# Kernel optimization log

Hardware: AMD Instinct MI355X
Metric: run time of the kernel (lower is better)

Reference implementation:

```python
import jax, jax.numpy as jnp
import numpy as np

N_EMBD = 768
N_HEAD = 12
HEAD_DIM = N_EMBD // N_HEAD
EPS = 1e-6


def setup_inputs() -> dict:
    key = jax.random.key(0)
    ks = jax.random.split(key, 8)
    B, T, C = 4, 2048, N_EMBD
    s = 0.02
    return {
        "x": jax.random.normal(ks[0], (B, T, C), jnp.float32),
        "ln1_w": jnp.ones((C,), jnp.float32),
        "ln1_b": jnp.zeros((C,), jnp.float32),
        "W_attn": jax.random.normal(ks[1], (C, 3 * C), jnp.float32) * s,
        "b_attn": jnp.zeros((3 * C,), jnp.float32),
        "W_attn_proj": jax.random.normal(ks[2], (C, C), jnp.float32) * s,
        "b_attn_proj": jnp.zeros((C,), jnp.float32),
        "ln2_w": jnp.ones((C,), jnp.float32),
        "ln2_b": jnp.zeros((C,), jnp.float32),
        "W_fc": jax.random.normal(ks[3], (C, 4 * C), jnp.float32) * s,
        "b_fc": jnp.zeros((4 * C,), jnp.float32),
        "W_mlp_proj": jax.random.normal(ks[4], (4 * C, C), jnp.float32) * s,
        "b_mlp_proj": jnp.zeros((C,), jnp.float32),
    }


def layer_norm(x, w, b):
    # Faithful to MyLayerNorm: (x - mean) / (std + eps), std with ddof=0
    mean = jnp.mean(x, axis=-1, keepdims=True)
    std = jnp.sqrt(jnp.mean((x - mean) ** 2, axis=-1, keepdims=True))
    return w * (x - mean) / (std + EPS) + b


def attention(h, W_attn, b_attn, W_proj, b_proj):
    B, T, C = h.shape
    qkv = h @ W_attn + b_attn                      # [B,T,3C]
    q, k, v = jnp.split(qkv, 3, axis=-1)
    # [B,T,C] -> [B,H,T,D]
    def to_heads(t):
        return t.reshape(B, T, N_HEAD, HEAD_DIM).transpose(0, 2, 1, 3)
    q, k, v = to_heads(q), to_heads(k), to_heads(v)
    att = jnp.einsum("bhtd,bhsd->bhts", q, k) * (1.0 / np.sqrt(HEAD_DIM))
    causal = jnp.tril(jnp.ones((T, T), bool))[None, None]
    att = jnp.where(causal, att, -jnp.inf)
    att = jax.nn.softmax(att, axis=-1)
    y = jnp.einsum("bhts,bhsd->bhtd", att, v)      # [B,H,T,D]
    y = y.transpose(0, 2, 1, 3).reshape(B, T, C)
    return y @ W_proj + b_proj


def mlp(h, W_fc, b_fc, W_proj, b_proj):
    h = jax.nn.gelu(h @ W_fc + b_fc, approximate=False)
    return h @ W_proj + b_proj


def reference(x, ln1_w, ln1_b, W_attn, b_attn, W_attn_proj, b_attn_proj,
              ln2_w, ln2_b, W_fc, b_fc, W_mlp_proj, b_mlp_proj):
    x = x + attention(layer_norm(x, ln1_w, ln1_b), W_attn, b_attn, W_attn_proj, b_attn_proj)
    x = x + mlp(layer_norm(x, ln2_w, ln2_b), W_fc, b_fc, W_mlp_proj, b_mlp_proj)
    return x
```

## Files before the change

### kernel.cpp

```cpp
#include <hip/hip_runtime.h>
#include <hip/hip_bf16.h>
#include <math.h>

#define N_EMBD 768
#define N_HEAD 12
#define HEAD_DIM 64
#define TOKENS 8192
#define SEQ 2048
#define BATCH 4
#define NQT (SEQ / 64)

typedef __attribute__((ext_vector_type(8))) short short8;
typedef __attribute__((ext_vector_type(4))) short short4v;
typedef __attribute__((ext_vector_type(4))) float f32x4;

__device__ __forceinline__ short f2bf(float f) {
    unsigned u = __builtin_bit_cast(unsigned, f);
    unsigned r = (u + 0x7fffu + ((u >> 16) & 1u)) >> 16;
    return (short)r;
}
__device__ __forceinline__ short f2bf_fast(float f) {
    unsigned u = __builtin_bit_cast(unsigned, f);
    return (short)((u + 0x8000u) >> 16);
}

__device__ __forceinline__ float gelu_fast(float x) {
    float z = 1.5957691216057308f * x * (1.0f + 0.044715f * x * x);
    return x / (1.0f + __expf(-z));
}

__device__ __forceinline__ void gld16(const void* g, void* l) {
    __builtin_amdgcn_global_load_lds(
        (const __attribute__((address_space(1))) unsigned int*)g,
        (__attribute__((address_space(3))) unsigned int*)l, 16, 0, 0);
}

__global__ __launch_bounds__(256) void wT_all(
        const float* __restrict__ Wa, short* __restrict__ Ta,
        const float* __restrict__ Wp, short* __restrict__ Tp,
        const float* __restrict__ Wf, short* __restrict__ Tf,
        const float* __restrict__ Wm, short* __restrict__ Tm) {
    __shared__ float T[32][33];
    int id = blockIdx.x;
    const float* W; short* Wt; int K, N;
    if (id < 1728)      { W = Wa; Wt = Ta; K = 768;  N = 2304; }
    else if (id < 2304) { W = Wp; Wt = Tp; K = 768;  N = 768;  id -= 1728; }
    else if (id < 4608) { W = Wf; Wt = Tf; K = 768;  N = 3072; id -= 2304; }
    else                { W = Wm; Wt = Tm; K = 3072; N = 768;  id -= 4608; }
    int tn = N >> 5;
    int n0 = (id % tn) * 32, k0 = (id / tn) * 32;
    int c = threadIdx.x & 31, r0 = threadIdx.x >> 5;
#pragma unroll
    for (int i = 0; i < 32; i += 8)
        T[r0 + i][c] = W[(size_t)(k0 + r0 + i) * N + n0 + c];
    __syncthreads();
#pragma unroll
    for (int i = 0; i < 32; i += 8)
        Wt[(size_t)(n0 + r0 + i) * K + k0 + c] = f2bf(T[c][r0 + i]);
}

__global__ __launch_bounds__(256) void ln_bf_kernel(const float* __restrict__ x,
                                                    const float* __restrict__ w,
                                                    const float* __restrict__ b,
                                                    short* __restrict__ out) {
    int row = blockIdx.x * 4 + (threadIdx.x >> 6);
    int lane = threadIdx.x & 63;
    const float4* xr = (const float4*)(x + (size_t)row * N_EMBD);
    const float4* wr = (const float4*)w;
    const float4* br = (const float4*)b;

    float4 v[3];
#pragma unroll
    for (int i = 0; i < 3; ++i) v[i] = xr[lane + 64 * i];
    float s = 0.f;
#pragma unroll
    for (int i = 0; i < 3; ++i) s += v[i].x + v[i].y + v[i].z + v[i].w;
#pragma unroll
    for (int off = 1; off < 64; off <<= 1) s += __shfl_xor(s, off, 64);
    float mean = s * (1.f / 768.f);

    float var = 0.f;
#pragma unroll
    for (int i = 0; i < 3; ++i) {
        float a0 = v[i].x - mean, a1 = v[i].y - mean,
              a2 = v[i].z - mean, a3 = v[i].w - mean;
        var += a0 * a0 + a1 * a1 + a2 * a2 + a3 * a3;
    }
#pragma unroll
    for (int off = 1; off < 64; off <<= 1) var += __shfl_xor(var, off, 64);
    float inv = 1.f / (sqrtf(var * (1.f / 768.f)) + 1e-6f);

    short4v* yr = (short4v*)(out + (size_t)row * N_EMBD);
#pragma unroll
    for (int i = 0; i < 3; ++i) {
        float4 wv = wr[lane + 64 * i], bv = br[lane + 64 * i];
        short4v o;
        o[0] = f2bf(wv.x * (v[i].x - mean) * inv + bv.x);
        o[1] = f2bf(wv.y * (v[i].y - mean) * inv + bv.y);
        o[2] = f2bf(wv.z * (v[i].z - mean) * inv + bv.z);
        o[3] = f2bf(wv.w * (v[i].w - mean) * inv + bv.w);
        yr[lane + 64 * i] = o;
    }
}

template <int ACT, int RES, int OUTBF, int VOUT>
__global__ __launch_bounds__(256) void gemm_mfma(
        const short* __restrict__ A,
        const short* __restrict__ Bt,
        const float* __restrict__ bias,
        const float* __restrict__ res,
        void* __restrict__ outp,
        short* __restrict__ vt,
        int M, int N, int K) {
    __shared__ short As[8192];
    __shared__ short Bs[8192];
    int tid = threadIdx.x;
    int wave = tid >> 6, lane = tid & 63;
    int quad = lane >> 4, l15 = lane & 15;
    int m0 = blockIdx.x * 128, n0 = blockIdx.y * 128;
    int wm = wave >> 1, wn = wave & 1;
    int sr = lane >> 2, sc = (lane & 3) * 8;

    f32x4 acc[4][4];
#pragma unroll
    for (int i = 0; i < 4; ++i)
#pragma unroll
        for (int j = 0; j < 4; ++j) acc[i][j] = (f32x4){0.f, 0.f, 0.f, 0.f};

    const short* ag = A + (size_t)(m0 + wave * 32 + sr) * K + sc;
    const short* bg = Bt + (size_t)(n0 + wave * 32 + sr) * K + sc;
    int woff = wave * 1024;

    gld16(ag, &As[woff]);
    gld16(ag + (size_t)16 * K, &As[woff + 512]);
    gld16(bg, &Bs[woff]);
    gld16(bg + (size_t)16 * K, &Bs[woff + 512]);

    int nk = K >> 5;
    for (int it = 0; it < nk; ++it) {
        int cb = (it & 1) * 4096;
        __syncthreads();
        if (it + 1 < nk) {
            int nb = ((it + 1) & 1) * 4096 + woff;
            int kn = (it + 1) << 5;
            gld16(ag + kn, &As[nb]);
            gld16(ag + kn + (size_t)16 * K, &As[nb + 512]);
            gld16(bg + kn, &Bs[nb]);
            gld16(bg + kn + (size_t)16 * K, &Bs[nb + 512]);
        }
        short8 af[4], bfr[4];
#pragma unroll
        for (int mt = 0; mt < 4; ++mt)
            af[mt] = *(const short8*)&As[cb + (wm * 64 + mt * 16 + l15) * 32 + quad * 8];
#pragma unroll
        for (int nt = 0; nt < 4; ++nt)
            bfr[nt] = *(const short8*)&Bs[cb + (wn * 64 + nt * 16 + l15) * 32 + quad * 8];
#pragma unroll
        for (int mt = 0; mt < 4; ++mt)
#pragma unroll
            for (int nt = 0; nt < 4; ++nt)
                acc[mt][nt] = __builtin_amdgcn_mfma_f32_16x16x32_bf16(
                    af[mt], bfr[nt], acc[mt][nt], 0, 0, 0);
    }

    if (VOUT && n0 >= 1536) {
#pragma unroll
        for (int mt = 0; mt < 4; ++mt) {
            int row0 = m0 + wm * 64 + mt * 16 + quad * 4;
            int b = row0 >> 11, t0 = row0 & 2047;
#pragma unroll
            for (int nt = 0; nt < 4; ++nt) {
                int col = n0 + wn * 64 + nt * 16 + l15;
                int vcol = col - 1536;
                int bh = b * N_HEAD + (vcol >> 6);
                int d = vcol & 63;
                float bi = bias[col];
                short4v o;
#pragma unroll
                for (int r = 0; r < 4; ++r) o[r] = f2bf(acc[mt][nt][r] + bi);
                *(short4v*)&vt[((size_t)bh * 64 + d) * SEQ + t0] = o;
            }
        }
        return;
    }

#pragma unroll
    for (int mt = 0; mt < 4; ++mt) {
        int row0 = m0 + wm * 64 + mt * 16 + quad * 4;
#pragma unroll
        for (int nt = 0; nt < 4; ++nt) {
            int col = n0 + wn * 64 + nt * 16 + l15;
            float bi = bias[col];
#pragma unroll
            for (int r = 0; r < 4; ++r) {
                float v = acc[mt][nt][r] + bi;
                if (ACT == 1) v = gelu_fast(v);
                if (RES) v += res[(size_t)(row0 + r) * N + col];
                if (OUTBF) ((short*)outp)[(size_t)(row0 + r) * N + col] = f2bf(v);
                else       ((float*)outp)[(size_t)(row0 + r) * N + col] = v;
            }
        }
    }
}

template <int ACT, int RES, int OUTBF>
__global__ __launch_bounds__(256) void gemm_mfma_n64(
        const short* __restrict__ A,
        const short* __restrict__ Bt,
        const float* __restrict__ bias,
        const float* __restrict__ res,
        void* __restrict__ outp,
        int M, int N, int K) {
    __shared__ short As[8192];
    __shared__ short Bs[4096];
    int tid = threadIdx.x;
    int wave = tid >> 6, lane = tid & 63;
    int quad = lane >> 4, l15 = lane & 15;
    int m0 = blockIdx.x * 128, n0 = blockIdx.y * 64;
    int wm = wave >> 1, wn = wave & 1;
    int sr = lane >> 2, sc = (lane & 3) * 8;

    f32x4 acc[4][2];
#pragma unroll
    for (int i = 0; i < 4; ++i)
#pragma unroll
        for (int j = 0; j < 2; ++j) acc[i][j] = (f32x4){0.f, 0.f, 0.f, 0.f};

    const short* gptr[3];
    int loff[3];
    bool isa[3];
#pragma unroll
    for (int j = 0; j < 3; ++j) {
        int c = wave * 3 + j;
        if (c < 8) {
            gptr[j] = A + (size_t)(m0 + c * 16 + sr) * K + sc;
            loff[j] = c * 512; isa[j] = true;
        } else {
            gptr[j] = Bt + (size_t)(n0 + (c - 8) * 16 + sr) * K + sc;
            loff[j] = (c - 8) * 512; isa[j] = false;
        }
    }

#pragma unroll
    for (int j = 0; j < 3; ++j)
        gld16(gptr[j], isa[j] ? &As[loff[j]] : &Bs[loff[j]]);

    int nk = K >> 5;
    for (int it = 0; it < nk; ++it) {
        int cba = (it & 1) * 4096, cbb = (it & 1) * 2048;
        __syncthreads();
        if (it + 1 < nk) {
            int nba = ((it + 1) & 1) * 4096, nbb = ((it + 1) & 1) * 2048;
            int kn = (it + 1) << 5;
#pragma unroll
            for (int j = 0; j < 3; ++j)
                gld16(gptr[j] + kn, isa[j] ? &As[nba + loff[j]] : &Bs[nbb + loff[j]]);
        }
        short8 af[4], bfr[2];
#pragma unroll
        for (int mt = 0; mt < 4; ++mt)
            af[mt] = *(const short8*)&As[cba + (wm * 64 + mt * 16 + l15) * 32 + quad * 8];
#pragma unroll
        for (int nt = 0; nt < 2; ++nt)
            bfr[nt] = *(const short8*)&Bs[cbb + (wn * 32 + nt * 16 + l15) * 32 + quad * 8];
#pragma unroll
        for (int mt = 0; mt < 4; ++mt)
#pragma unroll
            for (int nt = 0; nt < 2; ++nt)
                acc[mt][nt] = __builtin_amdgcn_mfma_f32_16x16x32_bf16(
                    af[mt], bfr[nt], acc[mt][nt], 0, 0, 0);
    }

#pragma unroll
    for (int mt = 0; mt < 4; ++mt) {
        int row0 = m0 + wm * 64 + mt * 16 + quad * 4;
#pragma unroll
        for (int nt = 0; nt < 2; ++nt) {
            int col = n0 + wn * 32 + nt * 16 + l15;
            float bi = bias[col];
#pragma unroll
            for (int r = 0; r < 4; ++r) {
                float v = acc[mt][nt][r] + bi;
                if (ACT == 1) v = gelu_fast(v);
                if (RES) v += res[(size_t)(row0 + r) * N + col];
                if (OUTBF) ((short*)outp)[(size_t)(row0 + r) * N + col] = f2bf(v);
                else       ((float*)outp)[(size_t)(row0 + r) * N + col] = v;
            }
        }
    }
}

template <bool DIAG>
__device__ __forceinline__ void attn_kt(
        const short* __restrict__ Ks, const short* __restrict__ Vs,
        short* __restrict__ Ps, int cb,
        const short8* qf, short8 ones,
        f32x4* o, f32x4& lacc,
        int wave, int quad, int l15, int pswz) {
    f32x4 sacc[4];
#pragma unroll
    for (int nt = 0; nt < 4; ++nt) sacc[nt] = (f32x4){0.f, 0.f, 0.f, 0.f};
#pragma unroll
    for (int nt = 0; nt < 4; ++nt)
#pragma unroll
        for (int ks = 0; ks < 2; ++ks) {
            short8 kf = *(const short8*)&Ks[cb + ks * 2048 + (nt * 16 + l15) * 32 + quad * 8];
            sacc[nt] = __builtin_amdgcn_mfma_f32_16x16x32_bf16(qf[ks], kf, sacc[nt], 0, 0, 0);
        }

#pragma unroll
    for (int nt = 0; nt < 4; ++nt) {
        int scol = nt * 16 + l15;
        int base = (scol >> 5) * 2048 + (scol & 31);
#pragma unroll
        for (int r = 0; r < 4; ++r) {
            float p = exp2f(fmaf(sacc[nt][r], 0.18033688011112042f,
                                 -5.770780163555854f));
            if (DIAG && (scol > wave * 16 + quad * 4 + r)) p = 0.f;
            Ps[(base + (wave * 16 + quad * 4 + r) * 32) ^ (quad << 4)] = f2bf_fast(p);
        }
    }

    short8 pf0 = *(const short8*)&Ps[((wave * 16 + l15) * 32 + quad * 8) ^ pswz];
    short8 pf1 = *(const short8*)&Ps[(2048 + (wave * 16 + l15) * 32 + quad * 8) ^ pswz];
    lacc = __builtin_amdgcn_mfma_f32_16x16x32_bf16(pf0, ones, lacc, 0, 0, 0);
    lacc = __builtin_amdgcn_mfma_f32_16x16x32_bf16(pf1, ones, lacc, 0, 0, 0);
#pragma unroll
    for (int nt = 0; nt < 4; ++nt) {
        short8 vf0 = *(const short8*)&Vs[cb + (nt * 16 + l15) * 32 + quad * 8];
        short8 vf1 = *(const short8*)&Vs[cb + 2048 + (nt * 16 + l15) * 32 + quad * 8];
        o[nt] = __builtin_amdgcn_mfma_f32_16x16x32_bf16(pf0, vf0, o[nt], 0, 0, 0);
        o[nt] = __builtin_amdgcn_mfma_f32_16x16x32_bf16(pf1, vf1, o[nt], 0, 0, 0);
    }
}

__device__ __forceinline__ void attn_tile(
        const short* __restrict__ qkv, const short* __restrict__ Vt,
        short* __restrict__ y, int bh, int qt,
        short* Ks, short* Vs, short* Ps) {
    int tid = threadIdx.x;
    int wave = tid >> 6, lane = tid & 63;
    int quad = lane >> 4, l15 = lane & 15;
    int h = bh % N_HEAD, b = bh / N_HEAD;
    size_t bT = (size_t)b * SEQ;
    int q0 = qt * 64;
    int sr = lane >> 2, sc = (lane & 3) * 8;

    const short ONE_BF = (short)0x3F80;
    short8 ones;
#pragma unroll
    for (int j = 0; j < 8; ++j) ones[j] = ONE_BF;

    const short* qrow = qkv + (bT + q0 + wave * 16 + l15) * 2304 + h * 64 + quad * 8;
    short8 qf[2];
    qf[0] = *(const short8*)qrow;
    qf[1] = *(const short8*)(qrow + 32);

    __syncthreads();
#pragma unroll
    for (int j = 0; j < 4; ++j) {
        int c = wave * 4 + j;
        if (c < 8) {
            int sub = c >> 2, r0 = (c & 3) * 16;
            const short* g = qkv + (bT + r0 + sr) * 2304 + 768 + h * 64 + sub * 32 + sc;
            gld16(g, &Ks[sub * 2048 + r0 * 32]);
        } else {
            int cv = c - 8;
            int sub = cv >> 2, r0 = (cv & 3) * 16;
            const short* g = Vt + ((size_t)bh * 64 + r0 + sr) * SEQ + sub * 32 + sc;
            gld16(g, &Vs[sub * 2048 + r0 * 32]);
        }
    }
    __syncthreads();

    f32x4 o[4];
#pragma unroll
    for (int nt = 0; nt < 4; ++nt) o[nt] = (f32x4){0.f, 0.f, 0.f, 0.f};
    f32x4 lacc = (f32x4){0.f, 0.f, 0.f, 0.f};

    const int pswz = ((l15 >> 2) & 3) << 4;

    for (int kt = 0; kt < qt; ++kt) {
        int cb = (kt & 1) * 4096;
        if (kt) __syncthreads();
        int nb = ((kt + 1) & 1) * 4096;
        int k0n = (kt + 1) * 64;
#pragma unroll
        for (int j = 0; j < 4; ++j) {
            int c = wave * 4 + j;
            if (c < 8) {
                int sub = c >> 2, r0 = (c & 3) * 16;
                const short* g = qkv + (bT + k0n + r0 + sr) * 2304 + 768 + h * 64 + sub * 32 + sc;
                gld16(g, &Ks[nb + sub * 2048 + r0 * 32]);
            } else {
                int cv = c - 8;
                int sub = cv >> 2, r0 = (cv & 3) * 16;
                const short* g = Vt + ((size_t)bh * 64 + r0 + sr) * SEQ + k0n + sub * 32 + sc;
                gld16(g, &Vs[nb + sub * 2048 + r0 * 32]);
            }
        }
        attn_kt<false>(Ks, Vs, Ps, cb, qf, ones, o, lacc, wave, quad, l15, pswz);
    }

    if (qt) __syncthreads();
    attn_kt<true>(Ks, Vs, Ps, (qt & 1) * 4096, qf, ones, o, lacc,
                  wave, quad, l15, pswz);

    float inv[4];
#pragma unroll
    for (int r = 0; r < 4; ++r) inv[r] = 1.f / lacc[r];
#pragma unroll
    for (int nt = 0; nt < 4; ++nt)
#pragma unroll
        for (int r = 0; r < 4; ++r)
            y[(bT + q0 + wave * 16 + quad * 4 + r) * N_EMBD + h * 64 + nt * 16 + l15] =
                f2bf(o[nt][r] * inv[r]);
}

__global__ __launch_bounds__(256, 4) void attn_mfma(
        const short* __restrict__ qkv, const short* __restrict__ Vt,
        short* __restrict__ y) {
    __shared__ short Ks[8192], Vs[8192], Ps[4096];
    int bh = blockIdx.x;
    int pair = blockIdx.y;
    attn_tile(qkv, Vt, y, bh, pair, Ks, Vs, Ps);
    attn_tile(qkv, Vt, y, bh, NQT - 1 - pair, Ks, Vs, Ps);
}

extern "C" void kernel_launch(void* const* d_in, const int* in_sizes, int n_in,
                              void* d_out, int out_size, void* d_ws, size_t ws_size,
                              hipStream_t stream) {
    const float* x         = (const float*)d_in[0];
    const float* ln1_w     = (const float*)d_in[1];
    const float* ln1_b     = (const float*)d_in[2];
    const float* W_attn    = (const float*)d_in[3];
    const float* b_attn    = (const float*)d_in[4];
    const float* W_attn_pr = (const float*)d_in[5];
    const float* b_attn_pr = (const float*)d_in[6];
    const float* ln2_w     = (const float*)d_in[7];
    const float* ln2_b     = (const float*)d_in[8];
    const float* W_fc      = (const float*)d_in[9];
    const float* b_fc      = (const float*)d_in[10];
    const float* W_mlp_pr  = (const float*)d_in[11];
    const float* b_mlp_pr  = (const float*)d_in[12];
    float* out = (float*)d_out;

    const int M = TOKENS, C = N_EMBD;
    char* ws = (char*)d_ws;
    size_t region0 = (size_t)M * 3072 * 2;
    short* qkv_bf = (short*)ws;
    short* fc_bf  = (short*)ws;
    size_t off = region0;
    short* VtB   = (short*)(ws + off); off += (size_t)48 * 64 * SEQ * 2;
    short* yb    = (short*)(ws + off); off += (size_t)M * C * 2;
    short* lnb   = (short*)(ws + off); off += (size_t)M * C * 2;
    float* x1    = (float*)(ws + off); off += (size_t)M * C * 4;
    short* WaT   = (short*)(ws + off); off += (size_t)2304 * 768 * 2;
    short* WpT   = (short*)(ws + off); off += (size_t)768 * 768 * 2;
    short* WfT   = (short*)(ws + off); off += (size_t)3072 * 768 * 2;
    short* WmT   = (short*)(ws + off); off += (size_t)768 * 3072 * 2;

    wT_all<<<6912, 256, 0, stream>>>(W_attn, WaT, W_attn_pr, WpT,
                                     W_fc, WfT, W_mlp_pr, WmT);

    ln_bf_kernel<<<M / 4, 256, 0, stream>>>(x, ln1_w, ln1_b, lnb);

    gemm_mfma<0, 0, 1, 1><<<dim3(M / 128, 2304 / 128), 256, 0, stream>>>(
        lnb, WaT, b_attn, nullptr, qkv_bf, VtB, M, 2304, 768);

    attn_mfma<<<dim3(BATCH * N_HEAD, NQT / 2), 256, 0, stream>>>(qkv_bf, VtB, yb);

    gemm_mfma_n64<0, 1, 0><<<dim3(M / 128, 768 / 64), 256, 0, stream>>>(
        yb, WpT, b_attn_pr, x, x1, M, 768, 768);

    ln_bf_kernel<<<M / 4, 256, 0, stream>>>(x1, ln2_w, ln2_b, lnb);

    gemm_mfma<1, 0, 1, 0><<<dim3(M / 128, 3072 / 128), 256, 0, stream>>>(
        lnb, WfT, b_fc, nullptr, fc_bf, nullptr, M, 3072, 768);

    gemm_mfma_n64<0, 1, 0><<<dim3(M / 128, 768 / 64), 256, 0, stream>>>(
        fc_bf, WmT, b_mlp_pr, x1, out, M, 768, 3072);
}
```

Baseline: 370.5 us.

## Swap MFMA operands for vectorized epilogues and keep attention P in registers

```diff
diff --git a/kernel.cpp b/kernel.cpp
--- a/kernel.cpp
+++ b/kernel.cpp
@@ -13,6 +13,7 @@
 typedef __attribute__((ext_vector_type(8))) short short8;
 typedef __attribute__((ext_vector_type(4))) short short4v;
 typedef __attribute__((ext_vector_type(4))) float f32x4;
+typedef __attribute__((ext_vector_type(4))) int int4v;
 
 __device__ __forceinline__ short f2bf(float f) {
     unsigned u = __builtin_bit_cast(unsigned, f);
@@ -22,6 +23,10 @@
 __device__ __forceinline__ short f2bf_fast(float f) {
     unsigned u = __builtin_bit_cast(unsigned, f);
     return (short)((u + 0x8000u) >> 16);
+}
+__device__ __forceinline__ unsigned pack2bf(float a, float b) {
+    return (unsigned)(unsigned short)f2bf_fast(a) |
+           ((unsigned)(unsigned short)f2bf_fast(b) << 16);
 }
 
 __device__ __forceinline__ float gelu_fast(float x) {
@@ -103,13 +108,12 @@
     }
 }
 
-template <int ACT, int RES, int OUTBF, int VOUT>
+template <int ACT, int VOUT, int SWAP>
 __global__ __launch_bounds__(256) void gemm_mfma(
         const short* __restrict__ A,
         const short* __restrict__ Bt,
         const float* __restrict__ bias,
-        const float* __restrict__ res,
-        void* __restrict__ outp,
+        short* __restrict__ outp,
         short* __restrict__ vt,
         int M, int N, int K) {
     __shared__ short As[8192];
@@ -158,9 +162,35 @@
 #pragma unroll
         for (int mt = 0; mt < 4; ++mt)
 #pragma unroll
-            for (int nt = 0; nt < 4; ++nt)
-                acc[mt][nt] = __builtin_amdgcn_mfma_f32_16x16x32_bf16(
-                    af[mt], bfr[nt], acc[mt][nt], 0, 0, 0);
+            for (int nt = 0; nt < 4; ++nt) {
+                if (SWAP)
+                    acc[mt][nt] = __builtin_amdgcn_mfma_f32_16x16x32_bf16(
+                        bfr[nt], af[mt], acc[mt][nt], 0, 0, 0);
+                else
+                    acc[mt][nt] = __builtin_amdgcn_mfma_f32_16x16x32_bf16(
+                        af[mt], bfr[nt], acc[mt][nt], 0, 0, 0);
+            }
+    }
+
+    if (SWAP) {
+#pragma unroll
+        for (int nt = 0; nt < 4; ++nt) {
+            int colb = n0 + wn * 64 + nt * 16 + quad * 4;
+            f32x4 b4 = *(const f32x4*)&bias[colb];
+#pragma unroll
+            for (int mt = 0; mt < 4; ++mt) {
+                int row = m0 + wm * 64 + mt * 16 + l15;
+                short4v o4;
+#pragma unroll
+                for (int r = 0; r < 4; ++r) {
+                    float v = acc[mt][nt][r] + b4[r];
+                    if (ACT) v = gelu_fast(v);
+                    o4[r] = f2bf(v);
+                }
+                *(short4v*)&outp[(size_t)row * N + colb] = o4;
+            }
+        }
+        return;
     }
 
     if (VOUT && n0 >= 1536) {
@@ -194,22 +224,19 @@
 #pragma unroll
             for (int r = 0; r < 4; ++r) {
                 float v = acc[mt][nt][r] + bi;
-                if (ACT == 1) v = gelu_fast(v);
-                if (RES) v += res[(size_t)(row0 + r) * N + col];
-                if (OUTBF) ((short*)outp)[(size_t)(row0 + r) * N + col] = f2bf(v);
-                else       ((float*)outp)[(size_t)(row0 + r) * N + col] = v;
+                if (ACT) v = gelu_fast(v);
+                outp[(size_t)(row0 + r) * N + col] = f2bf(v);
             }
         }
     }
 }
 
-template <int ACT, int RES, int OUTBF>
 __global__ __launch_bounds__(256) void gemm_mfma_n64(
         const short* __restrict__ A,
         const short* __restrict__ Bt,
         const float* __restrict__ bias,
         const float* __restrict__ res,
-        void* __restrict__ outp,
+        float* __restrict__ outp,
         int M, int N, int K) {
     __shared__ short As[8192];
     __shared__ short Bs[4096];
@@ -268,35 +295,30 @@
 #pragma unroll
             for (int nt = 0; nt < 2; ++nt)
                 acc[mt][nt] = __builtin_amdgcn_mfma_f32_16x16x32_bf16(
-                    af[mt], bfr[nt], acc[mt][nt], 0, 0, 0);
-    }
-
-#pragma unroll
-    for (int mt = 0; mt < 4; ++mt) {
-        int row0 = m0 + wm * 64 + mt * 16 + quad * 4;
-#pragma unroll
-        for (int nt = 0; nt < 2; ++nt) {
-            int col = n0 + wn * 32 + nt * 16 + l15;
-            float bi = bias[col];
-#pragma unroll
-            for (int r = 0; r < 4; ++r) {
-                float v = acc[mt][nt][r] + bi;
-                if (ACT == 1) v = gelu_fast(v);
-                if (RES) v += res[(size_t)(row0 + r) * N + col];
-                if (OUTBF) ((short*)outp)[(size_t)(row0 + r) * N + col] = f2bf(v);
-                else       ((float*)outp)[(size_t)(row0 + r) * N + col] = v;
-            }
+                    bfr[nt], af[mt], acc[mt][nt], 0, 0, 0);
+    }
+
+#pragma unroll
+    for (int nt = 0; nt < 2; ++nt) {
+        int colb = n0 + wn * 32 + nt * 16 + quad * 4;
+        f32x4 b4 = *(const f32x4*)&bias[colb];
+#pragma unroll
+        for (int mt = 0; mt < 4; ++mt) {
+            int row = m0 + wm * 64 + mt * 16 + l15;
+            f32x4 rv = *(const f32x4*)&res[(size_t)row * N + colb];
+            f32x4 ov;
+#pragma unroll
+            for (int r = 0; r < 4; ++r) ov[r] = acc[mt][nt][r] + b4[r] + rv[r];
+            *(f32x4*)&outp[(size_t)row * N + colb] = ov;
         }
     }
 }
 
 template <bool DIAG>
 __device__ __forceinline__ void attn_kt(
-        const short* __restrict__ Ks, const short* __restrict__ Vs,
-        short* __restrict__ Ps, int cb,
-        const short8* qf, short8 ones,
-        f32x4* o, f32x4& lacc,
-        int wave, int quad, int l15, int pswz) {
+        const short* __restrict__ Ks, const short* __restrict__ Vs, int cb,
+        const short8* qf, f32x4* o, float& lsum,
+        int wave, int quad, int l15) {
     f32x4 sacc[4];
 #pragma unroll
     for (int nt = 0; nt < 4; ++nt) sacc[nt] = (f32x4){0.f, 0.f, 0.f, 0.f};
@@ -305,39 +327,59 @@
 #pragma unroll
         for (int ks = 0; ks < 2; ++ks) {
             short8 kf = *(const short8*)&Ks[cb + ks * 2048 + (nt * 16 + l15) * 32 + quad * 8];
-            sacc[nt] = __builtin_amdgcn_mfma_f32_16x16x32_bf16(qf[ks], kf, sacc[nt], 0, 0, 0);
-        }
-
+            sacc[nt] = __builtin_amdgcn_mfma_f32_16x16x32_bf16(kf, qf[ks], sacc[nt], 0, 0, 0);
+        }
+
+    int qlt = wave * 16 + l15;
+    unsigned pk0[4], pk1[4];
 #pragma unroll
     for (int nt = 0; nt < 4; ++nt) {
-        int scol = nt * 16 + l15;
-        int base = (scol >> 5) * 2048 + (scol & 31);
+        float pv[4];
 #pragma unroll
         for (int r = 0; r < 4; ++r) {
+            int ls = nt * 16 + quad * 4 + r;
             float p = exp2f(fmaf(sacc[nt][r], 0.18033688011112042f,
                                  -5.770780163555854f));
-            if (DIAG && (scol > wave * 16 + quad * 4 + r)) p = 0.f;
-            Ps[(base + (wave * 16 + quad * 4 + r) * 32) ^ (quad << 4)] = f2bf_fast(p);
-        }
-    }
-
-    short8 pf0 = *(const short8*)&Ps[((wave * 16 + l15) * 32 + quad * 8) ^ pswz];
-    short8 pf1 = *(const short8*)&Ps[(2048 + (wave * 16 + l15) * 32 + quad * 8) ^ pswz];
-    lacc = __builtin_amdgcn_mfma_f32_16x16x32_bf16(pf0, ones, lacc, 0, 0, 0);
-    lacc = __builtin_amdgcn_mfma_f32_16x16x32_bf16(pf1, ones, lacc, 0, 0, 0);
-#pragma unroll
-    for (int nt = 0; nt < 4; ++nt) {
-        short8 vf0 = *(const short8*)&Vs[cb + (nt * 16 + l15) * 32 + quad * 8];
-        short8 vf1 = *(const short8*)&Vs[cb + 2048 + (nt * 16 + l15) * 32 + quad * 8];
-        o[nt] = __builtin_amdgcn_mfma_f32_16x16x32_bf16(pf0, vf0, o[nt], 0, 0, 0);
-        o[nt] = __builtin_amdgcn_mfma_f32_16x16x32_bf16(pf1, vf1, o[nt], 0, 0, 0);
+            if (DIAG && (ls > qlt)) p = 0.f;
+            pv[r] = p;
+            lsum += p;
+        }
+        pk0[nt] = pack2bf(pv[0], pv[1]);
+        pk1[nt] = pack2bf(pv[2], pv[3]);
+    }
+
+    int addrA = ((((2 * quad) & 3) << 4) + l15) << 2;
+    int addrB = ((((2 * quad + 1) & 3) << 4) + l15) << 2;
+    bool hi = quad >= 2;
+#pragma unroll
+    for (int ks = 0; ks < 2; ++ks) {
+        int nA = 2 * ks, nB = 2 * ks + 1;
+        int a0 = __builtin_amdgcn_ds_bpermute(addrA, (int)pk0[nA]);
+        int b0 = __builtin_amdgcn_ds_bpermute(addrA, (int)pk0[nB]);
+        int a1 = __builtin_amdgcn_ds_bpermute(addrA, (int)pk1[nA]);
+        int b1 = __builtin_amdgcn_ds_bpermute(addrA, (int)pk1[nB]);
+        int a2 = __builtin_amdgcn_ds_bpermute(addrB, (int)pk0[nA]);
+        int b2 = __builtin_amdgcn_ds_bpermute(addrB, (int)pk0[nB]);
+        int a3 = __builtin_amdgcn_ds_bpermute(addrB, (int)pk1[nA]);
+        int b3 = __builtin_amdgcn_ds_bpermute(addrB, (int)pk1[nB]);
+        int4v w;
+        w[0] = hi ? b0 : a0;
+        w[1] = hi ? b1 : a1;
+        w[2] = hi ? b2 : a2;
+        w[3] = hi ? b3 : a3;
+        short8 pf = __builtin_bit_cast(short8, w);
+#pragma unroll
+        for (int nt = 0; nt < 4; ++nt) {
+            short8 vf = *(const short8*)&Vs[cb + ks * 2048 + (nt * 16 + l15) * 32 + quad * 8];
+            o[nt] = __builtin_amdgcn_mfma_f32_16x16x32_bf16(vf, pf, o[nt], 0, 0, 0);
+        }
     }
 }
 
 __device__ __forceinline__ void attn_tile(
         const short* __restrict__ qkv, const short* __restrict__ Vt,
         short* __restrict__ y, int bh, int qt,
-        short* Ks, short* Vs, short* Ps) {
+        short* Ks, short* Vs) {
     int tid = threadIdx.x;
     int wave = tid >> 6, lane = tid & 63;
     int quad = lane >> 4, l15 = lane & 15;
@@ -345,11 +387,6 @@
     size_t bT = (size_t)b * SEQ;
     int q0 = qt * 64;
     int sr = lane >> 2, sc = (lane & 3) * 8;
-
-    const short ONE_BF = (short)0x3F80;
-    short8 ones;
-#pragma unroll
-    for (int j = 0; j < 8; ++j) ones[j] = ONE_BF;
 
     const short* qrow = qkv + (bT + q0 + wave * 16 + l15) * 2304 + h * 64 + quad * 8;
     short8 qf[2];
@@ -376,9 +413,7 @@
     f32x4 o[4];
 #pragma unroll
     for (int nt = 0; nt < 4; ++nt) o[nt] = (f32x4){0.f, 0.f, 0.f, 0.f};
-    f32x4 lacc = (f32x4){0.f, 0.f, 0.f, 0.f};
-
-    const int pswz = ((l15 >> 2) & 3) << 4;
+    float lsum = 0.f;
 
     for (int kt = 0; kt < qt; ++kt) {
         int cb = (kt & 1) * 4096;
@@ -399,32 +434,34 @@
                 gld16(g, &Vs[nb + sub * 2048 + r0 * 32]);
             }
         }
-        attn_kt<false>(Ks, Vs, Ps, cb, qf, ones, o, lacc, wave, quad, l15, pswz);
+        attn_kt<false>(Ks, Vs, cb, qf, o, lsum, wave, quad, l15);
     }
 
     if (qt) __syncthreads();
-    attn_kt<true>(Ks, Vs, Ps, (qt & 1) * 4096, qf, ones, o, lacc,
-                  wave, quad, l15, pswz);
-
-    float inv[4];
-#pragma unroll
-    for (int r = 0; r < 4; ++r) inv[r] = 1.f / lacc[r];
-#pragma unroll
-    for (int nt = 0; nt < 4; ++nt)
-#pragma unroll
-        for (int r = 0; r < 4; ++r)
-            y[(bT + q0 + wave * 16 + quad * 4 + r) * N_EMBD + h * 64 + nt * 16 + l15] =
-                f2bf(o[nt][r] * inv[r]);
+    attn_kt<true>(Ks, Vs, (qt & 1) * 4096, qf, o, lsum, wave, quad, l15);
+
+    lsum += __shfl_xor(lsum, 16, 64);
+    lsum += __shfl_xor(lsum, 32, 64);
+    float inv = 1.f / lsum;
+
+    short* yrow = y + (bT + q0 + wave * 16 + l15) * N_EMBD + h * 64;
+#pragma unroll
+    for (int nt = 0; nt < 4; ++nt) {
+        short4v yv;
+#pragma unroll
+        for (int r = 0; r < 4; ++r) yv[r] = f2bf(o[nt][r] * inv);
+        *(short4v*)&yrow[nt * 16 + quad * 4] = yv;
+    }
 }
 
 __global__ __launch_bounds__(256, 4) void attn_mfma(
         const short* __restrict__ qkv, const short* __restrict__ Vt,
         short* __restrict__ y) {
-    __shared__ short Ks[8192], Vs[8192], Ps[4096];
+    __shared__ short Ks[8192], Vs[8192];
     int bh = blockIdx.x;
     int pair = blockIdx.y;
-    attn_tile(qkv, Vt, y, bh, pair, Ks, Vs, Ps);
-    attn_tile(qkv, Vt, y, bh, NQT - 1 - pair, Ks, Vs, Ps);
+    attn_tile(qkv, Vt, y, bh, pair, Ks, Vs);
+    attn_tile(qkv, Vt, y, bh, NQT - 1 - pair, Ks, Vs);
 }
 
 extern "C" void kernel_launch(void* const* d_in, const int* in_sizes, int n_in,
@@ -465,19 +502,19 @@
 
     ln_bf_kernel<<<M / 4, 256, 0, stream>>>(x, ln1_w, ln1_b, lnb);
 
-    gemm_mfma<0, 0, 1, 1><<<dim3(M / 128, 2304 / 128), 256, 0, stream>>>(
-        lnb, WaT, b_attn, nullptr, qkv_bf, VtB, M, 2304, 768);
+    gemm_mfma<0, 1, 0><<<dim3(M / 128, 2304 / 128), 256, 0, stream>>>(
+        lnb, WaT, b_attn, qkv_bf, VtB, M, 2304, 768);
 
     attn_mfma<<<dim3(BATCH * N_HEAD, NQT / 2), 256, 0, stream>>>(qkv_bf, VtB, yb);
 
-    gemm_mfma_n64<0, 1, 0><<<dim3(M / 128, 768 / 64), 256, 0, stream>>>(
+    gemm_mfma_n64<<<dim3(M / 128, 768 / 64), 256, 0, stream>>>(
         yb, WpT, b_attn_pr, x, x1, M, 768, 768);
 
     ln_bf_kernel<<<M / 4, 256, 0, stream>>>(x1, ln2_w, ln2_b, lnb);
 
-    gemm_mfma<1, 0, 1, 0><<<dim3(M / 128, 3072 / 128), 256, 0, stream>>>(
-        lnb, WfT, b_fc, nullptr, fc_bf, nullptr, M, 3072, 768);
-
-    gemm_mfma_n64<0, 1, 0><<<dim3(M / 128, 768 / 64), 256, 0, stream>>>(
+    gemm_mfma<1, 0, 1><<<dim3(M / 128, 3072 / 128), 256, 0, stream>>>(
+        lnb, WfT, b_fc, fc_bf, nullptr, M, 3072, 768);
+
+    gemm_mfma_n64<<<dim3(M / 128, 768 / 64), 256, 0, stream>>>(
         fc_bf, WmT, b_mlp_pr, x1, out, M, 768, 3072);
 }
```

Measured after the change: 384.3 us. +3.7%, slower.

## Pipeline GEMM loads two stages ahead and vectorize epilogue via swapped MFMA operands

Applied to the files above, without the earlier changes.

```diff
diff --git a/kernel.cpp b/kernel.cpp
--- a/kernel.cpp
+++ b/kernel.cpp
@@ -103,13 +103,12 @@
     }
 }
 
-template <int ACT, int RES, int OUTBF, int VOUT>
+template <int ACT, int VOUT, int SWAP>
 __global__ __launch_bounds__(256) void gemm_mfma(
         const short* __restrict__ A,
         const short* __restrict__ Bt,
         const float* __restrict__ bias,
-        const float* __restrict__ res,
-        void* __restrict__ outp,
+        short* __restrict__ outp,
         short* __restrict__ vt,
         int M, int N, int K) {
     __shared__ short As[8192];
@@ -130,24 +129,26 @@
     const short* ag = A + (size_t)(m0 + wave * 32 + sr) * K + sc;
     const short* bg = Bt + (size_t)(n0 + wave * 32 + sr) * K + sc;
     int woff = wave * 1024;
-
-    gld16(ag, &As[woff]);
-    gld16(ag + (size_t)16 * K, &As[woff + 512]);
-    gld16(bg, &Bs[woff]);
-    gld16(bg + (size_t)16 * K, &Bs[woff + 512]);
-
     int nk = K >> 5;
+
+    auto stage = [&](int t) {
+        int nb = (t & 1) * 4096 + woff;
+        int kn = t << 5;
+        gld16(ag + kn, &As[nb]);
+        gld16(ag + kn + (size_t)16 * K, &As[nb + 512]);
+        gld16(bg + kn, &Bs[nb]);
+        gld16(bg + kn + (size_t)16 * K, &Bs[nb + 512]);
+    };
+
+    stage(0);
+    if (nk > 1) stage(1);
+
     for (int it = 0; it < nk; ++it) {
+        if (it + 1 < nk) asm volatile("s_waitcnt vmcnt(4)" ::: "memory");
+        else             asm volatile("s_waitcnt vmcnt(0)" ::: "memory");
+        __builtin_amdgcn_s_barrier();
+        __builtin_amdgcn_sched_barrier(0);
         int cb = (it & 1) * 4096;
-        __syncthreads();
-        if (it + 1 < nk) {
-            int nb = ((it + 1) & 1) * 4096 + woff;
-            int kn = (it + 1) << 5;
-            gld16(ag + kn, &As[nb]);
-            gld16(ag + kn + (size_t)16 * K, &As[nb + 512]);
-            gld16(bg + kn, &Bs[nb]);
-            gld16(bg + kn + (size_t)16 * K, &Bs[nb + 512]);
-        }
         short8 af[4], bfr[4];
 #pragma unroll
         for (int mt = 0; mt < 4; ++mt)
@@ -155,12 +156,45 @@
 #pragma unroll
         for (int nt = 0; nt < 4; ++nt)
             bfr[nt] = *(const short8*)&Bs[cb + (wn * 64 + nt * 16 + l15) * 32 + quad * 8];
+        asm volatile("s_waitcnt lgkmcnt(0)" ::: "memory");
+        __builtin_amdgcn_sched_barrier(0);
+        __builtin_amdgcn_s_setprio(1);
 #pragma unroll
         for (int mt = 0; mt < 4; ++mt)
 #pragma unroll
-            for (int nt = 0; nt < 4; ++nt)
-                acc[mt][nt] = __builtin_amdgcn_mfma_f32_16x16x32_bf16(
-                    af[mt], bfr[nt], acc[mt][nt], 0, 0, 0);
+            for (int nt = 0; nt < 4; ++nt) {
+                if (SWAP)
+                    acc[mt][nt] = __builtin_amdgcn_mfma_f32_16x16x32_bf16(
+                        bfr[nt], af[mt], acc[mt][nt], 0, 0, 0);
+                else
+                    acc[mt][nt] = __builtin_amdgcn_mfma_f32_16x16x32_bf16(
+                        af[mt], bfr[nt], acc[mt][nt], 0, 0, 0);
+            }
+        __builtin_amdgcn_s_setprio(0);
+        __builtin_amdgcn_sched_barrier(0);
+        __builtin_amdgcn_s_barrier();
+        if (it + 2 < nk) stage(it + 2);
+    }
+
+    if (SWAP) {
+#pragma unroll
+        for (int nt = 0; nt < 4; ++nt) {
+            int colb = n0 + wn * 64 + nt * 16 + quad * 4;
+            f32x4 b4 = *(const f32x4*)&bias[colb];
+#pragma unroll
+            for (int mt = 0; mt < 4; ++mt) {
+                int row = m0 + wm * 64 + mt * 16 + l15;
+                short4v o4;
+#pragma unroll
+                for (int r = 0; r < 4; ++r) {
+                    float v = acc[mt][nt][r] + b4[r];
+                    if (ACT) v = gelu_fast(v);
+                    o4[r] = f2bf(v);
+                }
+                *(short4v*)&outp[(size_t)row * N + colb] = o4;
+            }
+        }
+        return;
     }
 
     if (VOUT && n0 >= 1536) {
@@ -194,22 +228,19 @@
 #pragma unroll
             for (int r = 0; r < 4; ++r) {
                 float v = acc[mt][nt][r] + bi;
-                if (ACT == 1) v = gelu_fast(v);
-                if (RES) v += res[(size_t)(row0 + r) * N + col];
-                if (OUTBF) ((short*)outp)[(size_t)(row0 + r) * N + col] = f2bf(v);
-                else       ((float*)outp)[(size_t)(row0 + r) * N + col] = v;
+                if (ACT) v = gelu_fast(v);
+                outp[(size_t)(row0 + r) * N + col] = f2bf(v);
             }
         }
     }
 }
 
-template <int ACT, int RES, int OUTBF>
 __global__ __launch_bounds__(256) void gemm_mfma_n64(
         const short* __restrict__ A,
         const short* __restrict__ Bt,
         const float* __restrict__ bias,
         const float* __restrict__ res,
-        void* __restrict__ outp,
+        float* __restrict__ outp,
         int M, int N, int K) {
     __shared__ short As[8192];
     __shared__ short Bs[4096];
@@ -240,22 +271,25 @@
             loff[j] = (c - 8) * 512; isa[j] = false;
         }
     }
-
-#pragma unroll
-    for (int j = 0; j < 3; ++j)
-        gld16(gptr[j], isa[j] ? &As[loff[j]] : &Bs[loff[j]]);
-
     int nk = K >> 5;
+
+    auto stage = [&](int t) {
+        int nba = (t & 1) * 4096, nbb = (t & 1) * 2048;
+        int kn = t << 5;
+#pragma unroll
+        for (int j = 0; j < 3; ++j)
+            gld16(gptr[j] + kn, isa[j] ? &As[nba + loff[j]] : &Bs[nbb + loff[j]]);
+    };
+
+    stage(0);
+    if (nk > 1) stage(1);
+
     for (int it = 0; it < nk; ++it) {
+        if (it + 1 < nk) asm volatile("s_waitcnt vmcnt(3)" ::: "memory");
+        else             asm volatile("s_waitcnt vmcnt(0)" ::: "memory");
+        __builtin_amdgcn_s_barrier();
+        __builtin_amdgcn_sched_barrier(0);
         int cba = (it & 1) * 4096, cbb = (it & 1) * 2048;
-        __syncthreads();
-        if (it + 1 < nk) {
-            int nba = ((it + 1) & 1) * 4096, nbb = ((it + 1) & 1) * 2048;
-            int kn = (it + 1) << 5;
-#pragma unroll
-            for (int j = 0; j < 3; ++j)
-                gld16(gptr[j] + kn, isa[j] ? &As[nba + loff[j]] : &Bs[nbb + loff[j]]);
-        }
         short8 af[4], bfr[2];
 #pragma unroll
         for (int mt = 0; mt < 4; ++mt)
@@ -263,29 +297,33 @@
 #pragma unroll
         for (int nt = 0; nt < 2; ++nt)
             bfr[nt] = *(const short8*)&Bs[cbb + (wn * 32 + nt * 16 + l15) * 32 + quad * 8];
+        asm volatile("s_waitcnt lgkmcnt(0)" ::: "memory");
+        __builtin_amdgcn_sched_barrier(0);
+        __builtin_amdgcn_s_setprio(1);
 #pragma unroll
         for (int mt = 0; mt < 4; ++mt)
 #pragma unroll
             for (int nt = 0; nt < 2; ++nt)
                 acc[mt][nt] = __builtin_amdgcn_mfma_f32_16x16x32_bf16(
-                    af[mt], bfr[nt], acc[mt][nt], 0, 0, 0);
-    }
-
-#pragma unroll
-    for (int mt = 0; mt < 4; ++mt) {
-        int row0 = m0 + wm * 64 + mt * 16 + quad * 4;
-#pragma unroll
-        for (int nt = 0; nt < 2; ++nt) {
-            int col = n0 + wn * 32 + nt * 16 + l15;
-            float bi = bias[col];
-#pragma unroll
-            for (int r = 0; r < 4; ++r) {
-                float v = acc[mt][nt][r] + bi;
-                if (ACT == 1) v = gelu_fast(v);
-                if (RES) v += res[(size_t)(row0 + r) * N + col];
-                if (OUTBF) ((short*)outp)[(size_t)(row0 + r) * N + col] = f2bf(v);
-                else       ((float*)outp)[(size_t)(row0 + r) * N + col] = v;
-            }
+                    bfr[nt], af[mt], acc[mt][nt], 0, 0, 0);
+        __builtin_amdgcn_s_setprio(0);
+        __builtin_amdgcn_sched_barrier(0);
+        __builtin_amdgcn_s_barrier();
+        if (it + 2 < nk) stage(it + 2);
+    }
+
+#pragma unroll
+    for (int nt = 0; nt < 2; ++nt) {
+        int colb = n0 + wn * 32 + nt * 16 + quad * 4;
+        f32x4 b4 = *(const f32x4*)&bias[colb];
+#pragma unroll
+        for (int mt = 0; mt < 4; ++mt) {
+            int row = m0 + wm * 64 + mt * 16 + l15;
+            f32x4 rv = *(const f32x4*)&res[(size_t)row * N + colb];
+            f32x4 ov;
+#pragma unroll
+            for (int r = 0; r < 4; ++r) ov[r] = acc[mt][nt][r] + b4[r] + rv[r];
+            *(f32x4*)&outp[(size_t)row * N + colb] = ov;
         }
     }
 }
@@ -465,19 +503,19 @@
 
     ln_bf_kernel<<<M / 4, 256, 0, stream>>>(x, ln1_w, ln1_b, lnb);
 
-    gemm_mfma<0, 0, 1, 1><<<dim3(M / 128, 2304 / 128), 256, 0, stream>>>(
-        lnb, WaT, b_attn, nullptr, qkv_bf, VtB, M, 2304, 768);
+    gemm_mfma<0, 1, 0><<<dim3(M / 128, 2304 / 128), 256, 0, stream>>>(
+        lnb, WaT, b_attn, qkv_bf, VtB, M, 2304, 768);
 
     attn_mfma<<<dim3(BATCH * N_HEAD, NQT / 2), 256, 0, stream>>>(qkv_bf, VtB, yb);
 
-    gemm_mfma_n64<0, 1, 0><<<dim3(M / 128, 768 / 64), 256, 0, stream>>>(
+    gemm_mfma_n64<<<dim3(M / 128, 768 / 64), 256, 0, stream>>>(
         yb, WpT, b_attn_pr, x, x1, M, 768, 768);
 
     ln_bf_kernel<<<M / 4, 256, 0, stream>>>(x1, ln2_w, ln2_b, lnb);
 
-    gemm_mfma<1, 0, 1, 0><<<dim3(M / 128, 3072 / 128), 256, 0, stream>>>(
-        lnb, WfT, b_fc, nullptr, fc_bf, nullptr, M, 3072, 768);
-
-    gemm_mfma_n64<0, 1, 0><<<dim3(M / 128, 768 / 64), 256, 0, stream>>>(
+    gemm_mfma<1, 0, 1><<<dim3(M / 128, 3072 / 128), 256, 0, stream>>>(
+        lnb, WfT, b_fc, fc_bf, nullptr, M, 3072, 768);
+
+    gemm_mfma_n64<<<dim3(M / 128, 768 / 64), 256, 0, stream>>>(
         fc_bf, WmT, b_mlp_pr, x1, out, M, 768, 3072);
 }
```

After: 389.7 us. 5.2% more time.
